# Performance work log

Measured on AMD Instinct MI355X. Metric: run time of the kernel, lower is better.

Reference implementation:

```python
import jax, jax.numpy as jnp
import numpy as np

N = 50000          # nodes
E = 1_600_000      # edges (avg degree 32)
IN = 128           # in_channels
H = 2              # heads
C = 64             # out_channels per head


def setup_inputs() -> dict:
    key = jax.random.key(0)
    k = jax.random.split(key, 6)
    x = jax.random.normal(k[0], (N, IN), dtype=jnp.float32)
    edge_index = jax.random.randint(k[1], (2, E), 0, N, dtype=jnp.int32)
    W = jax.random.normal(k[2], (IN, H * C), dtype=jnp.float32) / np.sqrt(IN).astype(np.float32)
    att_src = jax.random.normal(k[3], (H, C), dtype=jnp.float32) * 0.1
    att_dst = jax.random.normal(k[4], (H, C), dtype=jnp.float32) * 0.1
    bias = jnp.zeros((C,), dtype=jnp.float32)
    return {"x": x, "W": W, "att_src": att_src, "att_dst": att_dst,
            "bias": bias, "edge_index": edge_index}


def reference(x, W, att_src, att_dst, bias, edge_index):
    Nn = x.shape[0]
    # linear projection per head: [N, H, C]
    h = (x @ W).reshape(Nn, H, C)
    # PyG GATConv default: add self loops
    loops = jnp.arange(Nn, dtype=edge_index.dtype)
    src = jnp.concatenate([edge_index[0], loops])  # [E+N]
    dst = jnp.concatenate([edge_index[1], loops])
    # per-node attention logits: a_src . h, a_dst . h -> [N, H]
    a_s = jnp.sum(h * att_src, axis=-1)
    a_d = jnp.sum(h * att_dst, axis=-1)
    # per-edge score, leaky relu (slope 0.2)
    e = jax.nn.leaky_relu(a_s[src] + a_d[dst], 0.2)  # [E+N, H]
    # softmax over incoming edges per destination node
    emax = jax.lax.stop_gradient(jax.ops.segment_max(e, dst, num_segments=Nn))
    e = jnp.exp(e - emax[dst])
    esum = jax.ops.segment_sum(e, dst, num_segments=Nn)
    alpha = e / (esum[dst] + 1e-16)                  # [E+N, H]
    # attention-weighted message passing: scatter-sum to destinations
    out = jax.ops.segment_sum(h[src] * alpha[:, :, None], dst, num_segments=Nn)  # [N, H, C]
    # concat=False -> mean over heads, then bias
    return out.mean(axis=1) + bias  # [N, C]
```

## Files before the change

### kernel.cpp

```cpp
#include <hip/hip_runtime.h>
#include <hip/hip_bf16.h>


#define NBLK 256
#define TH 512
#define BSH 7
#define BSZ 128
#define MAXBUCK 512
#define PLCAP 8192

typedef __attribute__((ext_vector_type(8))) short bf16x8;
typedef __attribute__((ext_vector_type(4))) float f32x4;

__device__ __forceinline__ ushort f2bf(float f) {
  __hip_bfloat16 b = __float2bfloat16(f);
  union { __hip_bfloat16 b; ushort u; } cv; cv.b = b; return cv.u;
}
__device__ __forceinline__ uint pk2(float a, float b) {
  return (uint)f2bf(a) | ((uint)f2bf(b) << 16);
}

__global__ __launch_bounds__(128) void k_wa(const float* __restrict__ W,
                                            const float* __restrict__ as,
                                            const float* __restrict__ ad,
                                            ushort* __restrict__ wa) {
  const int k = threadIdx.x;
  float s0 = 0.f, s1 = 0.f, d0 = 0.f, d1 = 0.f;
  const float* wr = &W[k * 128];
  for (int c = 0; c < 64; ++c) {
    float w0 = wr[c], w1 = wr[64 + c];
    s0 = fmaf(w0, as[c], s0);
    s1 = fmaf(w1, as[64 + c], s1);
    d0 = fmaf(w0, ad[c], d0);
    d1 = fmaf(w1, ad[64 + c], d1);
  }
  wa[k * 4 + 0] = f2bf(s0);
  wa[k * 4 + 1] = f2bf(s1);
  wa[k * 4 + 2] = f2bf(d0);
  wa[k * 4 + 3] = f2bf(d1);
}

__global__ __launch_bounds__(256) void k_gemm(
    const float* __restrict__ x, const float* __restrict__ W,
    const ushort* __restrict__ wa, __hip_bfloat162* __restrict__ h2,
    float* __restrict__ a_s, float* __restrict__ a_d, int Nn) {
  __shared__ ushort Al[64 * 128];
  char* lb = (char*)Al;
  const int wave = threadIdx.x >> 6;
  const int lane = threadIdx.x & 63;
  const int row0 = blockIdx.x * 64;
  const int l15 = lane & 15;
  const int kb = (lane >> 4) * 8;

  {
    const int t = threadIdx.x;
    const int srow = t >> 2, q = t & 3;
    int gr = row0 + srow; gr = (gr < Nn) ? gr : (Nn - 1);
    const float4* xr = (const float4*)&x[(size_t)gr * 128 + q * 32];
#pragma unroll
    for (int i = 0; i < 4; ++i) {
      float4 v0 = xr[2 * i], v1 = xr[2 * i + 1];
      uint4 w;
      w.x = pk2(v0.x, v0.y); w.y = pk2(v0.z, v0.w);
      w.z = pk2(v1.x, v1.y); w.w = pk2(v1.z, v1.w);
      int byte = srow * 256 + ((q * 64 + i * 16) ^ ((srow & 7) << 4));
      *(uint4*)(lb + byte) = w;
    }
  }

  bf16x8 bfr[2][4];
#pragma unroll
  for (int c = 0; c < 2; ++c) {
#pragma unroll
    for (int ks = 0; ks < 4; ++ks) {
      const float* wp = &W[(ks * 32 + kb) * 128 + wave * 32 + c * 16 + l15];
      union { bf16x8 v; ushort u[8]; } t;
#pragma unroll
      for (int j = 0; j < 8; ++j) t.u[j] = f2bf(wp[j * 128]);
      bfr[c][ks] = t.v;
    }
  }
  bf16x8 wafr[4];
  if (wave == 3) {
#pragma unroll
    for (int ks = 0; ks < 4; ++ks) {
      union { bf16x8 v; ushort u[8]; } t;
#pragma unroll
      for (int j = 0; j < 8; ++j)
        t.u[j] = (l15 < 4) ? wa[(ks * 32 + kb + j) * 4 + l15] : (ushort)0;
      wafr[ks] = t.v;
    }
  }

  __syncthreads();

  f32x4 acc[4][2];
  f32x4 accwa[4];
#pragma unroll
  for (int r = 0; r < 4; ++r) {
    acc[r][0] = (f32x4){0.f, 0.f, 0.f, 0.f};
    acc[r][1] = (f32x4){0.f, 0.f, 0.f, 0.f};
    accwa[r] = (f32x4){0.f, 0.f, 0.f, 0.f};
  }
#pragma unroll
  for (int ks = 0; ks < 4; ++ks) {
    bf16x8 af[4];
#pragma unroll
    for (int r = 0; r < 4; ++r) {
      int row = r * 16 + l15;
      int byte = row * 256 + ((ks * 64 + (lane >> 4) * 16) ^ ((row & 7) << 4));
      uint4 v = *(const uint4*)(lb + byte);
      union { uint4 q; bf16x8 v; } cv; cv.q = v;
      af[r] = cv.v;
    }
#pragma unroll
    for (int r = 0; r < 4; ++r) {
      acc[r][0] = __builtin_amdgcn_mfma_f32_16x16x32_bf16(af[r], bfr[0][ks],
                                                          acc[r][0], 0, 0, 0);
      acc[r][1] = __builtin_amdgcn_mfma_f32_16x16x32_bf16(af[r], bfr[1][ks],
                                                          acc[r][1], 0, 0, 0);
    }
    if (wave == 3) {
#pragma unroll
      for (int r = 0; r < 4; ++r)
        accwa[r] = __builtin_amdgcn_mfma_f32_16x16x32_bf16(af[r], wafr[ks],
                                                           accwa[r], 0, 0, 0);
    }
  }

  ushort* hs = (ushort*)h2;
  const int rbase = (lane >> 4) * 4;
#pragma unroll
  for (int r = 0; r < 4; ++r) {
#pragma unroll
    for (int c = 0; c < 2; ++c) {
      int col = wave * 32 + c * 16 + l15;
#pragma unroll
      for (int i = 0; i < 4; ++i) {
        int grow = row0 + r * 16 + rbase + i;
        if (grow < Nn) hs[(size_t)grow * 128 + col] = f2bf(acc[r][c][i]);
      }
    }
  }
  if (wave == 3) {
#pragma unroll
    for (int r = 0; r < 4; ++r) {
#pragma unroll
      for (int i = 0; i < 4; ++i) {
        int grow = row0 + r * 16 + rbase + i;
        if (grow < Nn) {
          float v = accwa[r][i];
          if (l15 < 2) a_s[grow * 2 + l15] = v;
          else if (l15 < 4) a_d[grow * 2 + (l15 - 2)] = v;
        }
      }
    }
  }
}

__global__ __launch_bounds__(TH) void k_bhist(const int* __restrict__ dst,
                                              int* __restrict__ bhist, int E,
                                              int nbuck, int chunk) {
  __shared__ int hl[MAXBUCK];
  for (int i = threadIdx.x; i < nbuck; i += TH) hl[i] = 0;
  __syncthreads();
  const int s = blockIdx.x * chunk;
  const int e = (s + chunk < E) ? s + chunk : E;
  for (int i = s + threadIdx.x; i < e; i += TH)
    atomicAdd(&hl[dst[i] >> BSH], 1);
  __syncthreads();
  for (int b = threadIdx.x; b < nbuck; b += TH)
    bhist[b * NBLK + blockIdx.x] = hl[b];
}

__global__ __launch_bounds__(NBLK) void k_bscan(const int* __restrict__ bhist,
                                                int* __restrict__ cursors,
                                                int* __restrict__ totals,
                                                int nbuck) {
  __shared__ int tmp[NBLK];
  const int b = blockIdx.x;
  const int t = threadIdx.x;
  const int v = bhist[b * NBLK + t];
  tmp[t] = v;
  __syncthreads();
  for (int d = 1; d < NBLK; d <<= 1) {
    int add = (t >= d) ? tmp[t - d] : 0;
    __syncthreads();
    tmp[t] += add;
    __syncthreads();
  }
  cursors[t * nbuck + b] = tmp[t] - v;
  if (t == NBLK - 1) totals[b] = tmp[t];
}

__global__ __launch_bounds__(MAXBUCK) void k_bbase(const int* __restrict__ totals,
                                                   int* __restrict__ bases,
                                                   int nbuck) {
  __shared__ int tmp[MAXBUCK];
  const int t = threadIdx.x;
  const int v = (t < nbuck) ? totals[t] : 0;
  tmp[t] = v;
  __syncthreads();
  for (int d = 1; d < MAXBUCK; d <<= 1) {
    int add = (t >= d) ? tmp[t - d] : 0;
    __syncthreads();
    tmp[t] += add;
    __syncthreads();
  }
  if (t < nbuck) bases[t] = tmp[t] - v;
  if (t == nbuck - 1) bases[nbuck] = tmp[t];
}

__global__ __launch_bounds__(TH) void k_binsert(
    const int* __restrict__ src, const int* __restrict__ dst,
    const int* __restrict__ cursors, const int* __restrict__ bases,
    int* __restrict__ pairs, int E, int nbuck, int chunk) {
  __shared__ int cur[MAXBUCK];
  for (int i = threadIdx.x; i < nbuck; i += TH)
    cur[i] = cursors[blockIdx.x * nbuck + i] + bases[i];
  __syncthreads();
  const int s = blockIdx.x * chunk;
  const int e = (s + chunk < E) ? s + chunk : E;
  for (int i = s + threadIdx.x; i < e; i += TH) {
    const int d = dst[i];
    const int b = d >> BSH;
    const int p = atomicAdd(&cur[b], 1);
    pairs[p] = ((d & (BSZ - 1)) << 16) | src[i];
  }
}

__global__ __launch_bounds__(256) void k_bucket(
    const int* __restrict__ pairs, const int* __restrict__ bases,
    int* __restrict__ off, int* __restrict__ cnt, int* __restrict__ csr,
    int Nn) {
  __shared__ int pl[PLCAP];
  __shared__ int cl[BSZ];
  __shared__ int tmp[BSZ];
  __shared__ int cu[BSZ];
  const int b = blockIdx.x;
  const int t = threadIdx.x;
  const int n0 = b << BSH;
  if (t < BSZ) cl[t] = 0;
  __syncthreads();
  const int s = bases[b], e = bases[b + 1];
  const int len = e - s;
  const bool fit = (len <= PLCAP);
  if (fit) {
    for (int i = t; i < len; i += 256) {
      int pv = pairs[s + i];
      pl[i] = pv;
      atomicAdd(&cl[pv >> 16], 1);
    }
  } else {
    for (int i = s + t; i < e; i += 256) atomicAdd(&cl[pairs[i] >> 16], 1);
  }
  __syncthreads();
  int v = 0;
  if (t < BSZ) { v = cl[t]; tmp[t] = v; }
  __syncthreads();
  for (int d = 1; d < BSZ; d <<= 1) {
    int add = (t < BSZ && t >= d) ? tmp[t - d] : 0;
    __syncthreads();
    if (t < BSZ) tmp[t] += add;
    __syncthreads();
  }
  if (t < BSZ) {
    const int excl = tmp[t] - v;
    cu[t] = s + excl;
    const int node = n0 + t;
    if (node < Nn) { off[node] = s + excl; cnt[node] = v; }
  }
  __syncthreads();
  if (fit) {
    for (int i = t; i < len; i += 256) {
      const int pv = pl[i];
      const int p = atomicAdd(&cu[pv >> 16], 1);
      csr[p] = pv & 0xffff;
    }
  } else {
    for (int i = s + t; i < e; i += 256) {
      const int pv = pairs[i];
      const int p = atomicAdd(&cu[pv >> 16], 1);
      csr[p] = pv & 0xffff;
    }
  }
}

__device__ __forceinline__ float leaky02(float v) {
  return fmaxf(v, 0.2f * v);
}

__global__ __launch_bounds__(256) void k_aggr(
    const __hip_bfloat162* __restrict__ h2, const float* __restrict__ a_s,
    const float* __restrict__ a_d, const int* __restrict__ off,
    const int* __restrict__ cnt, const int* __restrict__ csr,
    const float* __restrict__ bias, float* __restrict__ out, int Nn) {
  __shared__ uint2 ewA[4][64];
  __shared__ uint2 ewB[4][64];
  const int wave = threadIdx.x >> 6;
  const int lane = threadIdx.x & 63;
  const int d = blockIdx.x * 4 + wave;
  if (d >= Nn) return;
  const int o = off[d];
  const int deg = cnt[d];
  const float2 ad2 = *(const float2*)&a_d[d * 2];
  const char* hb = (const char*)h2;
  const unsigned l4 = lane * 4u;
  const uint4* ebase = (lane < 32) ? (const uint4*)&ewA[wave][0]
                                   : (const uint4*)&ewB[wave][0];

  float acc0 = 0.f, acc1 = 0.f;
  float sw0 = 0.f, sw1 = 0.f;

  for (int c = 0; c < deg; c += 64) {
    int rem = deg - c; if (rem > 64) rem = 64;
    {
      unsigned voff = 0; float w0 = 0.f, w1 = 0.f;
      if (lane < rem) {
        int sl = csr[o + c + lane];
        float2 as2 = *(const float2*)&a_s[sl * 2];
        w0 = __expf(leaky02(as2.x + ad2.x));
        w1 = __expf(leaky02(as2.y + ad2.y));
        voff = (unsigned)sl << 8;
        sw0 += w0; sw1 += w1;
      }
      ewA[wave][lane] = make_uint2(voff, __float_as_uint(w0));
      ewB[wave][lane] = make_uint2(voff, __float_as_uint(w1));
    }
    const int nq = (rem + 1) >> 1;
    int q = 0;
    for (; q + 4 <= nq; q += 4) {
      uint4 p0 = ebase[q + 0];
      uint4 p1 = ebase[q + 1];
      uint4 p2 = ebase[q + 2];
      uint4 p3 = ebase[q + 3];
      __hip_bfloat162 hA0 = *(const __hip_bfloat162*)(hb + (size_t)(p0.x + l4));
      __hip_bfloat162 hB0 = *(const __hip_bfloat162*)(hb + (size_t)(p0.z + l4));
      __hip_bfloat162 hA1 = *(const __hip_bfloat162*)(hb + (size_t)(p1.x + l4));
      __hip_bfloat162 hB1 = *(const __hip_bfloat162*)(hb + (size_t)(p1.z + l4));
      __hip_bfloat162 hA2 = *(const __hip_bfloat162*)(hb + (size_t)(p2.x + l4));
      __hip_bfloat162 hB2 = *(const __hip_bfloat162*)(hb + (size_t)(p2.z + l4));
      __hip_bfloat162 hA3 = *(const __hip_bfloat162*)(hb + (size_t)(p3.x + l4));
      __hip_bfloat162 hB3 = *(const __hip_bfloat162*)(hb + (size_t)(p3.z + l4));
      acc0 = fmaf(__uint_as_float(p0.y), __bfloat162float(hA0.x), acc0);
      acc1 = fmaf(__uint_as_float(p0.y), __bfloat162float(hA0.y), acc1);
      acc0 = fmaf(__uint_as_float(p0.w), __bfloat162float(hB0.x), acc0);
      acc1 = fmaf(__uint_as_float(p0.w), __bfloat162float(hB0.y), acc1);
      acc0 = fmaf(__uint_as_float(p1.y), __bfloat162float(hA1.x), acc0);
      acc1 = fmaf(__uint_as_float(p1.y), __bfloat162float(hA1.y), acc1);
      acc0 = fmaf(__uint_as_float(p1.w), __bfloat162float(hB1.x), acc0);
      acc1 = fmaf(__uint_as_float(p1.w), __bfloat162float(hB1.y), acc1);
      acc0 = fmaf(__uint_as_float(p2.y), __bfloat162float(hA2.x), acc0);
      acc1 = fmaf(__uint_as_float(p2.y), __bfloat162float(hA2.y), acc1);
      acc0 = fmaf(__uint_as_float(p2.w), __bfloat162float(hB2.x), acc0);
      acc1 = fmaf(__uint_as_float(p2.w), __bfloat162float(hB2.y), acc1);
      acc0 = fmaf(__uint_as_float(p3.y), __bfloat162float(hA3.x), acc0);
      acc1 = fmaf(__uint_as_float(p3.y), __bfloat162float(hA3.y), acc1);
      acc0 = fmaf(__uint_as_float(p3.w), __bfloat162float(hB3.x), acc0);
      acc1 = fmaf(__uint_as_float(p3.w), __bfloat162float(hB3.y), acc1);
    }
    for (; q < nq; ++q) {
      uint4 p = ebase[q];
      __hip_bfloat162 hA = *(const __hip_bfloat162*)(hb + (size_t)(p.x + l4));
      __hip_bfloat162 hB = *(const __hip_bfloat162*)(hb + (size_t)(p.z + l4));
      acc0 = fmaf(__uint_as_float(p.y), __bfloat162float(hA.x), acc0);
      acc1 = fmaf(__uint_as_float(p.y), __bfloat162float(hA.y), acc1);
      acc0 = fmaf(__uint_as_float(p.w), __bfloat162float(hB.x), acc0);
      acc1 = fmaf(__uint_as_float(p.w), __bfloat162float(hB.y), acc1);
    }
  }
#pragma unroll
  for (int msk = 1; msk <= 32; msk <<= 1) {
    sw0 += __shfl_xor(sw0, msk, 64);
    sw1 += __shfl_xor(sw1, msk, 64);
  }
  {
    float2 as2 = *(const float2*)&a_s[d * 2];
    float w0 = __expf(leaky02(as2.x + ad2.x));
    float w1 = __expf(leaky02(as2.y + ad2.y));
    sw0 += w0; sw1 += w1;
    float av = (lane < 32) ? w0 : w1;
    __hip_bfloat162 hv = h2[(size_t)d * 64 + lane];
    acc0 = fmaf(av, __bfloat162float(hv.x), acc0);
    acc1 = fmaf(av, __bfloat162float(hv.y), acc1);
  }
  const float invsel = 1.f / (((lane < 32) ? sw0 : sw1) + 1e-16f);
  acc0 *= invsel; acc1 *= invsel;
  float o0 = acc0 + __shfl_down(acc0, 32, 64);
  float o1 = acc1 + __shfl_down(acc1, 32, 64);
  if (lane < 32) {
    int c = lane * 2;
    float2 res = make_float2(0.5f * o0 + bias[c], 0.5f * o1 + bias[c + 1]);
    *(float2*)&out[(size_t)d * 64 + c] = res;
  }
}

extern "C" void kernel_launch(void* const* d_in, const int* in_sizes, int n_in,
                              void* d_out, int out_size, void* d_ws,
                              size_t ws_size, hipStream_t stream) {
  const float* x = (const float*)d_in[0];
  const float* W = (const float*)d_in[1];
  const float* att_s = (const float*)d_in[2];
  const float* att_d = (const float*)d_in[3];
  const float* bias = (const float*)d_in[4];
  const int* ei = (const int*)d_in[5];
  const int Nn = in_sizes[0] / 128;
  const int E = in_sizes[5] / 2;
  const int* src = ei;
  const int* dst = ei + E;
  float* out = (float*)d_out;

  const int nbuck = (Nn + BSZ - 1) >> BSH;
  const int chunk = (E + NBLK - 1) / NBLK;

  __hip_bfloat162* h2 = (__hip_bfloat162*)d_ws;
  float* a_s = (float*)(h2 + (size_t)Nn * 64);
  float* a_d = a_s + (size_t)Nn * 2;
  int* off = (int*)(a_d + (size_t)Nn * 2);
  int* cnt = off + Nn;
  int* bhist = cnt + Nn;
  int* cursors = bhist + (size_t)nbuck * NBLK;
  int* totals = cursors + (size_t)NBLK * nbuck;
  int* bases = totals + nbuck;
  ushort* wa = (ushort*)(bases + nbuck + 1);
  int* pairs = (int*)(wa + 512);
  int* csr = pairs + (size_t)E;

  hipLaunchKernelGGL(k_wa, dim3(1), dim3(128), 0, stream, W, att_s, att_d, wa);
  hipLaunchKernelGGL(k_gemm, dim3((Nn + 63) / 64), dim3(256), 0, stream, x, W,
                     wa, h2, a_s, a_d, Nn);
  hipLaunchKernelGGL(k_bhist, dim3(NBLK), dim3(TH), 0, stream, dst, bhist, E,
                     nbuck, chunk);
  hipLaunchKernelGGL(k_bscan, dim3(nbuck), dim3(NBLK), 0, stream, bhist,
                     cursors, totals, nbuck);
  hipLaunchKernelGGL(k_bbase, dim3(1), dim3(MAXBUCK), 0, stream, totals, bases,
                     nbuck);
  hipLaunchKernelGGL(k_binsert, dim3(NBLK), dim3(TH), 0, stream, src, dst,
                     cursors, bases, pairs, E, nbuck, chunk);
  hipLaunchKernelGGL(k_bucket, dim3(nbuck), dim3(256), 0, stream, pairs, bases,
                     off, cnt, csr, Nn);
  hipLaunchKernelGGL(k_aggr, dim3((Nn + 3) / 4), dim3(256), 0, stream, h2, a_s,
                     a_d, off, cnt, csr, bias, out, Nn);
}
```

Baseline: 117.8 us.

## Split aggregation into alpha precompute and column-split gather with atomic output

Replaces the single fused aggregation kernel with three kernels: an output init with bias, a kernel that computes normalized attention weights per edge (including the self loop) into two per-head edge arrays, and a gather kernel launched over four column quarters that accumulates weighted bf16 features and atomically adds into the output. The aim is more parallelism and memory-level concurrency in the gather, since each wave handles 4 edges at a time over 16-lane groups. The cost is extra global writes and reads of the edge weight arrays (16 bytes per edge), each edge's exp being computed twice, one more launch, and atomic adds on the output.

```diff
diff --git a/kernel.cpp b/kernel.cpp
--- a/kernel.cpp
+++ b/kernel.cpp
@@ -290,108 +290,110 @@
   return fmaxf(v, 0.2f * v);
 }
 
-__global__ __launch_bounds__(256) void k_aggr(
-    const __hip_bfloat162* __restrict__ h2, const float* __restrict__ a_s,
-    const float* __restrict__ a_d, const int* __restrict__ off,
-    const int* __restrict__ cnt, const int* __restrict__ csr,
-    const float* __restrict__ bias, float* __restrict__ out, int Nn) {
-  __shared__ uint2 ewA[4][64];
-  __shared__ uint2 ewB[4][64];
+__global__ __launch_bounds__(256) void k_init(float* __restrict__ out,
+                                              const float* __restrict__ bias,
+                                              int total) {
+  int i = blockIdx.x * 256 + threadIdx.x;
+  if (i < total) out[i] = bias[i & 63];
+}
+
+__global__ __launch_bounds__(256) void k_alpha(
+    const float* __restrict__ a_s, const float* __restrict__ a_d,
+    const int* __restrict__ off, const int* __restrict__ cnt,
+    const int* __restrict__ csr, uint2* __restrict__ ed0,
+    uint2* __restrict__ ed1, int Nn) {
   const int wave = threadIdx.x >> 6;
   const int lane = threadIdx.x & 63;
   const int d = blockIdx.x * 4 + wave;
   if (d >= Nn) return;
-  const int o = off[d];
-  const int deg = cnt[d];
+  const int o = off[d], deg = cnt[d];
+  const int o2 = o + d;
   const float2 ad2 = *(const float2*)&a_d[d * 2];
-  const char* hb = (const char*)h2;
-  const unsigned l4 = lane * 4u;
-  const uint4* ebase = (lane < 32) ? (const uint4*)&ewA[wave][0]
-                                   : (const uint4*)&ewB[wave][0];
-
-  float acc0 = 0.f, acc1 = 0.f;
   float sw0 = 0.f, sw1 = 0.f;
-
-  for (int c = 0; c < deg; c += 64) {
-    int rem = deg - c; if (rem > 64) rem = 64;
-    {
-      unsigned voff = 0; float w0 = 0.f, w1 = 0.f;
-      if (lane < rem) {
-        int sl = csr[o + c + lane];
-        float2 as2 = *(const float2*)&a_s[sl * 2];
-        w0 = __expf(leaky02(as2.x + ad2.x));
-        w1 = __expf(leaky02(as2.y + ad2.y));
-        voff = (unsigned)sl << 8;
-        sw0 += w0; sw1 += w1;
-      }
-      ewA[wave][lane] = make_uint2(voff, __float_as_uint(w0));
-      ewB[wave][lane] = make_uint2(voff, __float_as_uint(w1));
-    }
-    const int nq = (rem + 1) >> 1;
-    int q = 0;
-    for (; q + 4 <= nq; q += 4) {
-      uint4 p0 = ebase[q + 0];
-      uint4 p1 = ebase[q + 1];
-      uint4 p2 = ebase[q + 2];
-      uint4 p3 = ebase[q + 3];
-      __hip_bfloat162 hA0 = *(const __hip_bfloat162*)(hb + (size_t)(p0.x + l4));
-      __hip_bfloat162 hB0 = *(const __hip_bfloat162*)(hb + (size_t)(p0.z + l4));
-      __hip_bfloat162 hA1 = *(const __hip_bfloat162*)(hb + (size_t)(p1.x + l4));
-      __hip_bfloat162 hB1 = *(const __hip_bfloat162*)(hb + (size_t)(p1.z + l4));
-      __hip_bfloat162 hA2 = *(const __hip_bfloat162*)(hb + (size_t)(p2.x + l4));
-      __hip_bfloat162 hB2 = *(const __hip_bfloat162*)(hb + (size_t)(p2.z + l4));
-      __hip_bfloat162 hA3 = *(const __hip_bfloat162*)(hb + (size_t)(p3.x + l4));
-      __hip_bfloat162 hB3 = *(const __hip_bfloat162*)(hb + (size_t)(p3.z + l4));
-      acc0 = fmaf(__uint_as_float(p0.y), __bfloat162float(hA0.x), acc0);
-      acc1 = fmaf(__uint_as_float(p0.y), __bfloat162float(hA0.y), acc1);
-      acc0 = fmaf(__uint_as_float(p0.w), __bfloat162float(hB0.x), acc0);
-      acc1 = fmaf(__uint_as_float(p0.w), __bfloat162float(hB0.y), acc1);
-      acc0 = fmaf(__uint_as_float(p1.y), __bfloat162float(hA1.x), acc0);
-      acc1 = fmaf(__uint_as_float(p1.y), __bfloat162float(hA1.y), acc1);
-      acc0 = fmaf(__uint_as_float(p1.w), __bfloat162float(hB1.x), acc0);
-      acc1 = fmaf(__uint_as_float(p1.w), __bfloat162float(hB1.y), acc1);
-      acc0 = fmaf(__uint_as_float(p2.y), __bfloat162float(hA2.x), acc0);
-      acc1 = fmaf(__uint_as_float(p2.y), __bfloat162float(hA2.y), acc1);
-      acc0 = fmaf(__uint_as_float(p2.w), __bfloat162float(hB2.x), acc0);
-      acc1 = fmaf(__uint_as_float(p2.w), __bfloat162float(hB2.y), acc1);
-      acc0 = fmaf(__uint_as_float(p3.y), __bfloat162float(hA3.x), acc0);
-      acc1 = fmaf(__uint_as_float(p3.y), __bfloat162float(hA3.y), acc1);
-      acc0 = fmaf(__uint_as_float(p3.w), __bfloat162float(hB3.x), acc0);
-      acc1 = fmaf(__uint_as_float(p3.w), __bfloat162float(hB3.y), acc1);
-    }
-    for (; q < nq; ++q) {
-      uint4 p = ebase[q];
-      __hip_bfloat162 hA = *(const __hip_bfloat162*)(hb + (size_t)(p.x + l4));
-      __hip_bfloat162 hB = *(const __hip_bfloat162*)(hb + (size_t)(p.z + l4));
-      acc0 = fmaf(__uint_as_float(p.y), __bfloat162float(hA.x), acc0);
-      acc1 = fmaf(__uint_as_float(p.y), __bfloat162float(hA.y), acc1);
-      acc0 = fmaf(__uint_as_float(p.w), __bfloat162float(hB.x), acc0);
-      acc1 = fmaf(__uint_as_float(p.w), __bfloat162float(hB.y), acc1);
-    }
-  }
-#pragma unroll
-  for (int msk = 1; msk <= 32; msk <<= 1) {
-    sw0 += __shfl_xor(sw0, msk, 64);
-    sw1 += __shfl_xor(sw1, msk, 64);
-  }
-  {
-    float2 as2 = *(const float2*)&a_s[d * 2];
+  for (int e = lane; e < deg; e += 64) {
+    int sl = csr[o + e];
+    float2 as2 = *(const float2*)&a_s[sl * 2];
+    sw0 += __expf(leaky02(as2.x + ad2.x));
+    sw1 += __expf(leaky02(as2.y + ad2.y));
+  }
+#pragma unroll
+  for (int m = 1; m <= 32; m <<= 1) {
+    sw0 += __shfl_xor(sw0, m, 64);
+    sw1 += __shfl_xor(sw1, m, 64);
+  }
+  const float2 asd = *(const float2*)&a_s[d * 2];
+  const float ws0 = __expf(leaky02(asd.x + ad2.x));
+  const float ws1 = __expf(leaky02(asd.y + ad2.y));
+  const float inv0 = 1.f / (sw0 + ws0 + 1e-16f);
+  const float inv1 = 1.f / (sw1 + ws1 + 1e-16f);
+  for (int e = lane; e < deg; e += 64) {
+    int sl = csr[o + e];
+    float2 as2 = *(const float2*)&a_s[sl * 2];
     float w0 = __expf(leaky02(as2.x + ad2.x));
     float w1 = __expf(leaky02(as2.y + ad2.y));
-    sw0 += w0; sw1 += w1;
-    float av = (lane < 32) ? w0 : w1;
-    __hip_bfloat162 hv = h2[(size_t)d * 64 + lane];
-    acc0 = fmaf(av, __bfloat162float(hv.x), acc0);
-    acc1 = fmaf(av, __bfloat162float(hv.y), acc1);
-  }
-  const float invsel = 1.f / (((lane < 32) ? sw0 : sw1) + 1e-16f);
-  acc0 *= invsel; acc1 *= invsel;
-  float o0 = acc0 + __shfl_down(acc0, 32, 64);
-  float o1 = acc1 + __shfl_down(acc1, 32, 64);
-  if (lane < 32) {
-    int c = lane * 2;
-    float2 res = make_float2(0.5f * o0 + bias[c], 0.5f * o1 + bias[c + 1]);
-    *(float2*)&out[(size_t)d * 64 + c] = res;
+    ed0[o2 + e] = make_uint2((uint)sl << 8, __float_as_uint(w0 * inv0));
+    ed1[o2 + e] = make_uint2((uint)sl << 8, __float_as_uint(w1 * inv1));
+  }
+  if (lane == 0) {
+    ed0[o2 + deg] = make_uint2((uint)d << 8, __float_as_uint(ws0 * inv0));
+    ed1[o2 + deg] = make_uint2((uint)d << 8, __float_as_uint(ws1 * inv1));
+  }
+}
+
+__global__ __launch_bounds__(256) void k_gat(
+    const __hip_bfloat162* __restrict__ h2, const uint2* __restrict__ ed0,
+    const uint2* __restrict__ ed1, const int* __restrict__ off,
+    const int* __restrict__ cnt, float* __restrict__ out, int Nn) {
+  const int wave = threadIdx.x >> 6;
+  const int lane = threadIdx.x & 63;
+  const int d = blockIdx.x * 4 + wave;
+  if (d >= Nn) return;
+  const int c = blockIdx.y;
+  const uint2* __restrict__ ed = (c >> 1) ? ed1 : ed0;
+  const int n = cnt[d] + 1;
+  const int o2 = off[d] + d;
+  const char* hb = (const char*)h2;
+  const uint claneoff =
+      (uint)((c >> 1) * 128 + (c & 1) * 64 + (lane & 15) * 4);
+  const int g = lane >> 4;
+  float acc0 = 0.f, acc1 = 0.f;
+  int e = 0;
+  for (; e + 16 <= n; e += 16) {
+    uint2 e0 = ed[o2 + e + g];
+    uint2 e1 = ed[o2 + e + 4 + g];
+    uint2 e2 = ed[o2 + e + 8 + g];
+    uint2 e3 = ed[o2 + e + 12 + g];
+    uint v0 = *(const uint*)(hb + (size_t)(e0.x + claneoff));
+    uint v1 = *(const uint*)(hb + (size_t)(e1.x + claneoff));
+    uint v2 = *(const uint*)(hb + (size_t)(e2.x + claneoff));
+    uint v3 = *(const uint*)(hb + (size_t)(e3.x + claneoff));
+    float a0 = __uint_as_float(e0.y), a1 = __uint_as_float(e1.y);
+    float a2 = __uint_as_float(e2.y), a3 = __uint_as_float(e3.y);
+    acc0 = fmaf(a0, __uint_as_float(v0 << 16), acc0);
+    acc1 = fmaf(a0, __uint_as_float(v0 & 0xffff0000u), acc1);
+    acc0 = fmaf(a1, __uint_as_float(v1 << 16), acc0);
+    acc1 = fmaf(a1, __uint_as_float(v1 & 0xffff0000u), acc1);
+    acc0 = fmaf(a2, __uint_as_float(v2 << 16), acc0);
+    acc1 = fmaf(a2, __uint_as_float(v2 & 0xffff0000u), acc1);
+    acc0 = fmaf(a3, __uint_as_float(v3 << 16), acc0);
+    acc1 = fmaf(a3, __uint_as_float(v3 & 0xffff0000u), acc1);
+  }
+  for (; e < n; e += 4) {
+    int idx = e + g;
+    uint2 e0 = ed[o2 + ((idx < n) ? idx : n - 1)];
+    float a0 = (idx < n) ? __uint_as_float(e0.y) : 0.f;
+    uint v0 = *(const uint*)(hb + (size_t)(e0.x + claneoff));
+    acc0 = fmaf(a0, __uint_as_float(v0 << 16), acc0);
+    acc1 = fmaf(a0, __uint_as_float(v0 & 0xffff0000u), acc1);
+  }
+  acc0 += __shfl_xor(acc0, 16, 64);
+  acc0 += __shfl_xor(acc0, 32, 64);
+  acc1 += __shfl_xor(acc1, 16, 64);
+  acc1 += __shfl_xor(acc1, 32, 64);
+  if (lane < 16) {
+    float* op = &out[(size_t)d * 64 + (c & 1) * 32 + lane * 2];
+    atomicAdd(op, 0.5f * acc0);
+    atomicAdd(op + 1, 0.5f * acc1);
   }
 }
 
@@ -425,6 +427,10 @@
   ushort* wa = (ushort*)(bases + nbuck + 1);
   int* pairs = (int*)(wa + 512);
   int* csr = pairs + (size_t)E;
+  uint2* ed0 = (uint2*)(csr + (size_t)E);
+  uint2* ed1 = ed0 + (size_t)(E + Nn);
+
+  const int ndb = (Nn + 3) / 4;
 
   hipLaunchKernelGGL(k_wa, dim3(1), dim3(128), 0, stream, W, att_s, att_d, wa);
   hipLaunchKernelGGL(k_gemm, dim3((Nn + 63) / 64), dim3(256), 0, stream, x, W,
@@ -439,6 +445,10 @@
                      cursors, bases, pairs, E, nbuck, chunk);
   hipLaunchKernelGGL(k_bucket, dim3(nbuck), dim3(256), 0, stream, pairs, bases,
                      off, cnt, csr, Nn);
-  hipLaunchKernelGGL(k_aggr, dim3((Nn + 3) / 4), dim3(256), 0, stream, h2, a_s,
-                     a_d, off, cnt, csr, bias, out, Nn);
-}
+  hipLaunchKernelGGL(k_init, dim3((Nn * 64 + 255) / 256), dim3(256), 0, stream,
+                     out, bias, Nn * 64);
+  hipLaunchKernelGGL(k_alpha, dim3(ndb), dim3(256), 0, stream, a_s, a_d, off,
+                     cnt, csr, ed0, ed1, Nn);
+  hipLaunchKernelGGL(k_gat, dim3(ndb, 4), dim3(256), 0, stream, h2, ed0, ed1,
+                     off, cnt, out, Nn);
+}
```

Measured after the change: 204.9 us. 1.74x slower.

## Precompute normalized attention weights in bucket kernel and stream them into aggregation

Applied to the files above, without the earlier changes.

The per-edge softmax (exp, per-destination sum, reciprocal) moves into the bucketing kernel, which now writes 16-byte records holding the source offset and the normalized weights for both heads, with the self-loop included per node. The aggregation kernel then only streams these records and gathers h, with no a_s lookups, no exp and no cross-lane reductions. It also unrolls the gather by 8 and converts bf16 with bit shifts. The cost is a larger edge array (16 B per edge instead of 4 B written and read back) and a second pass over pairs in the bucket kernel that recomputes exp and issues shared-memory float atomics.

```diff
diff --git a/kernel.cpp b/kernel.cpp
--- a/kernel.cpp
+++ b/kernel.cpp
@@ -229,30 +229,44 @@
   }
 }
 
+__device__ __forceinline__ float leaky02(float v) {
+  return fmaxf(v, 0.2f * v);
+}
+
 __global__ __launch_bounds__(256) void k_bucket(
     const int* __restrict__ pairs, const int* __restrict__ bases,
-    int* __restrict__ off, int* __restrict__ cnt, int* __restrict__ csr,
+    const float* __restrict__ a_s, const float* __restrict__ a_d,
+    int* __restrict__ off, int* __restrict__ cnt, uint4* __restrict__ edAB,
     int Nn) {
   __shared__ int pl[PLCAP];
   __shared__ int cl[BSZ];
   __shared__ int tmp[BSZ];
   __shared__ int cu[BSZ];
+  __shared__ float es0[BSZ], es1[BSZ];
+  __shared__ float inv0l[BSZ], inv1l[BSZ];
+  __shared__ float adl0[BSZ], adl1[BSZ];
   const int b = blockIdx.x;
   const int t = threadIdx.x;
   const int n0 = b << BSH;
-  if (t < BSZ) cl[t] = 0;
+  if (t < BSZ) {
+    cl[t] = 0; es0[t] = 0.f; es1[t] = 0.f;
+    const int node = n0 + t;
+    float2 ad2 = make_float2(0.f, 0.f);
+    if (node < Nn) ad2 = *(const float2*)&a_d[node * 2];
+    adl0[t] = ad2.x; adl1[t] = ad2.y;
+  }
   __syncthreads();
   const int s = bases[b], e = bases[b + 1];
   const int len = e - s;
   const bool fit = (len <= PLCAP);
-  if (fit) {
-    for (int i = t; i < len; i += 256) {
-      int pv = pairs[s + i];
-      pl[i] = pv;
-      atomicAdd(&cl[pv >> 16], 1);
-    }
-  } else {
-    for (int i = s + t; i < e; i += 256) atomicAdd(&cl[pairs[i] >> 16], 1);
+  for (int i = t; i < len; i += 256) {
+    const int pv = pairs[s + i];
+    if (fit) pl[i] = pv;
+    const int ld = pv >> 16, sr = pv & 0xffff;
+    atomicAdd(&cl[ld], 1);
+    float2 as2 = *(const float2*)&a_s[sr * 2];
+    atomicAdd(&es0[ld], __expf(leaky02(as2.x + adl0[ld])));
+    atomicAdd(&es1[ld], __expf(leaky02(as2.y + adl1[ld])));
   }
   __syncthreads();
   int v = 0;
@@ -268,32 +282,37 @@
     const int excl = tmp[t] - v;
     cu[t] = s + excl;
     const int node = n0 + t;
-    if (node < Nn) { off[node] = s + excl; cnt[node] = v; }
-  }
-  __syncthreads();
-  if (fit) {
-    for (int i = t; i < len; i += 256) {
-      const int pv = pl[i];
-      const int p = atomicAdd(&cu[pv >> 16], 1);
-      csr[p] = pv & 0xffff;
-    }
-  } else {
-    for (int i = s + t; i < e; i += 256) {
-      const int pv = pairs[i];
-      const int p = atomicAdd(&cu[pv >> 16], 1);
-      csr[p] = pv & 0xffff;
-    }
-  }
-}
-
-__device__ __forceinline__ float leaky02(float v) {
-  return fmaxf(v, 0.2f * v);
+    if (node < Nn) {
+      off[node] = s + excl;
+      cnt[node] = v;
+      float2 asd = *(const float2*)&a_s[node * 2];
+      const float ws0 = __expf(leaky02(asd.x + adl0[t]));
+      const float ws1 = __expf(leaky02(asd.y + adl1[t]));
+      const float i0 = 1.f / (es0[t] + ws0 + 1e-16f);
+      const float i1 = 1.f / (es1[t] + ws1 + 1e-16f);
+      inv0l[t] = i0; inv1l[t] = i1;
+      const size_t sidx = (size_t)(s + excl + v) + node;
+      edAB[sidx] = make_uint4((uint)node << 8, __float_as_uint(ws0 * i0),
+                              (uint)node << 8, __float_as_uint(ws1 * i1));
+    }
+  }
+  __syncthreads();
+  for (int i = t; i < len; i += 256) {
+    const int pv = fit ? pl[i] : pairs[s + i];
+    const int ld = pv >> 16, sr = pv & 0xffff;
+    float2 as2 = *(const float2*)&a_s[sr * 2];
+    const float w0 = __expf(leaky02(as2.x + adl0[ld]));
+    const float w1 = __expf(leaky02(as2.y + adl1[ld]));
+    const int p = atomicAdd(&cu[ld], 1);
+    const size_t gi = (size_t)p + (n0 + ld);
+    edAB[gi] = make_uint4((uint)sr << 8, __float_as_uint(w0 * inv0l[ld]),
+                          (uint)sr << 8, __float_as_uint(w1 * inv1l[ld]));
+  }
 }
 
 __global__ __launch_bounds__(256) void k_aggr(
-    const __hip_bfloat162* __restrict__ h2, const float* __restrict__ a_s,
-    const float* __restrict__ a_d, const int* __restrict__ off,
-    const int* __restrict__ cnt, const int* __restrict__ csr,
+    const __hip_bfloat162* __restrict__ h2, const uint4* __restrict__ edAB,
+    const int* __restrict__ off, const int* __restrict__ cnt,
     const float* __restrict__ bias, float* __restrict__ out, int Nn) {
   __shared__ uint2 ewA[4][64];
   __shared__ uint2 ewB[4][64];
@@ -301,91 +320,54 @@
   const int lane = threadIdx.x & 63;
   const int d = blockIdx.x * 4 + wave;
   if (d >= Nn) return;
-  const int o = off[d];
-  const int deg = cnt[d];
-  const float2 ad2 = *(const float2*)&a_d[d * 2];
+  const int o2 = off[d] + d;
+  const int n = cnt[d] + 1;
   const char* hb = (const char*)h2;
   const unsigned l4 = lane * 4u;
   const uint4* ebase = (lane < 32) ? (const uint4*)&ewA[wave][0]
                                    : (const uint4*)&ewB[wave][0];
-
   float acc0 = 0.f, acc1 = 0.f;
-  float sw0 = 0.f, sw1 = 0.f;
-
-  for (int c = 0; c < deg; c += 64) {
-    int rem = deg - c; if (rem > 64) rem = 64;
+
+  for (int c = 0; c < n; c += 64) {
+    int rem = n - c; if (rem > 64) rem = 64;
     {
-      unsigned voff = 0; float w0 = 0.f, w1 = 0.f;
-      if (lane < rem) {
-        int sl = csr[o + c + lane];
-        float2 as2 = *(const float2*)&a_s[sl * 2];
-        w0 = __expf(leaky02(as2.x + ad2.x));
-        w1 = __expf(leaky02(as2.y + ad2.y));
-        voff = (unsigned)sl << 8;
-        sw0 += w0; sw1 += w1;
-      }
-      ewA[wave][lane] = make_uint2(voff, __float_as_uint(w0));
-      ewB[wave][lane] = make_uint2(voff, __float_as_uint(w1));
+      uint4 tld = make_uint4(0, 0, 0, 0);
+      if (lane < rem) tld = edAB[(size_t)o2 + c + lane];
+      ewA[wave][lane] = make_uint2(tld.x, tld.y);
+      ewB[wave][lane] = make_uint2(tld.z, tld.w);
     }
     const int nq = (rem + 1) >> 1;
     int q = 0;
-    for (; q + 4 <= nq; q += 4) {
-      uint4 p0 = ebase[q + 0];
-      uint4 p1 = ebase[q + 1];
-      uint4 p2 = ebase[q + 2];
-      uint4 p3 = ebase[q + 3];
-      __hip_bfloat162 hA0 = *(const __hip_bfloat162*)(hb + (size_t)(p0.x + l4));
-      __hip_bfloat162 hB0 = *(const __hip_bfloat162*)(hb + (size_t)(p0.z + l4));
-      __hip_bfloat162 hA1 = *(const __hip_bfloat162*)(hb + (size_t)(p1.x + l4));
-      __hip_bfloat162 hB1 = *(const __hip_bfloat162*)(hb + (size_t)(p1.z + l4));
-      __hip_bfloat162 hA2 = *(const __hip_bfloat162*)(hb + (size_t)(p2.x + l4));
-      __hip_bfloat162 hB2 = *(const __hip_bfloat162*)(hb + (size_t)(p2.z + l4));
-      __hip_bfloat162 hA3 = *(const __hip_bfloat162*)(hb + (size_t)(p3.x + l4));
-      __hip_bfloat162 hB3 = *(const __hip_bfloat162*)(hb + (size_t)(p3.z + l4));
-      acc0 = fmaf(__uint_as_float(p0.y), __bfloat162float(hA0.x), acc0);
-      acc1 = fmaf(__uint_as_float(p0.y), __bfloat162float(hA0.y), acc1);
-      acc0 = fmaf(__uint_as_float(p0.w), __bfloat162float(hB0.x), acc0);
-      acc1 = fmaf(__uint_as_float(p0.w), __bfloat162float(hB0.y), acc1);
-      acc0 = fmaf(__uint_as_float(p1.y), __bfloat162float(hA1.x), acc0);
-      acc1 = fmaf(__uint_as_float(p1.y), __bfloat162float(hA1.y), acc1);
-      acc0 = fmaf(__uint_as_float(p1.w), __bfloat162float(hB1.x), acc0);
-      acc1 = fmaf(__uint_as_float(p1.w), __bfloat162float(hB1.y), acc1);
-      acc0 = fmaf(__uint_as_float(p2.y), __bfloat162float(hA2.x), acc0);
-      acc1 = fmaf(__uint_as_float(p2.y), __bfloat162float(hA2.y), acc1);
-      acc0 = fmaf(__uint_as_float(p2.w), __bfloat162float(hB2.x), acc0);
-      acc1 = fmaf(__uint_as_float(p2.w), __bfloat162float(hB2.y), acc1);
-      acc0 = fmaf(__uint_as_float(p3.y), __bfloat162float(hA3.x), acc0);
-      acc1 = fmaf(__uint_as_float(p3.y), __bfloat162float(hA3.y), acc1);
-      acc0 = fmaf(__uint_as_float(p3.w), __bfloat162float(hB3.x), acc0);
-      acc1 = fmaf(__uint_as_float(p3.w), __bfloat162float(hB3.y), acc1);
+    for (; q + 8 <= nq; q += 8) {
+      uint4 p[8];
+#pragma unroll
+      for (int u = 0; u < 8; ++u) p[u] = ebase[q + u];
+      uint va[8], vb[8];
+#pragma unroll
+      for (int u = 0; u < 8; ++u) {
+        va[u] = *(const uint*)(hb + (size_t)(p[u].x + l4));
+        vb[u] = *(const uint*)(hb + (size_t)(p[u].z + l4));
+      }
+#pragma unroll
+      for (int u = 0; u < 8; ++u) {
+        const float aa = __uint_as_float(p[u].y);
+        const float ab = __uint_as_float(p[u].w);
+        acc0 = fmaf(aa, __uint_as_float(va[u] << 16), acc0);
+        acc1 = fmaf(aa, __uint_as_float(va[u] & 0xffff0000u), acc1);
+        acc0 = fmaf(ab, __uint_as_float(vb[u] << 16), acc0);
+        acc1 = fmaf(ab, __uint_as_float(vb[u] & 0xffff0000u), acc1);
+      }
     }
     for (; q < nq; ++q) {
       uint4 p = ebase[q];
-      __hip_bfloat162 hA = *(const __hip_bfloat162*)(hb + (size_t)(p.x + l4));
-      __hip_bfloat162 hB = *(const __hip_bfloat162*)(hb + (size_t)(p.z + l4));
-      acc0 = fmaf(__uint_as_float(p.y), __bfloat162float(hA.x), acc0);
-      acc1 = fmaf(__uint_as_float(p.y), __bfloat162float(hA.y), acc1);
-      acc0 = fmaf(__uint_as_float(p.w), __bfloat162float(hB.x), acc0);
-      acc1 = fmaf(__uint_as_float(p.w), __bfloat162float(hB.y), acc1);
-    }
-  }
-#pragma unroll
-  for (int msk = 1; msk <= 32; msk <<= 1) {
-    sw0 += __shfl_xor(sw0, msk, 64);
-    sw1 += __shfl_xor(sw1, msk, 64);
-  }
-  {
-    float2 as2 = *(const float2*)&a_s[d * 2];
-    float w0 = __expf(leaky02(as2.x + ad2.x));
-    float w1 = __expf(leaky02(as2.y + ad2.y));
-    sw0 += w0; sw1 += w1;
-    float av = (lane < 32) ? w0 : w1;
-    __hip_bfloat162 hv = h2[(size_t)d * 64 + lane];
-    acc0 = fmaf(av, __bfloat162float(hv.x), acc0);
-    acc1 = fmaf(av, __bfloat162float(hv.y), acc1);
-  }
-  const float invsel = 1.f / (((lane < 32) ? sw0 : sw1) + 1e-16f);
-  acc0 *= invsel; acc1 *= invsel;
+      uint va = *(const uint*)(hb + (size_t)(p.x + l4));
+      uint vb = *(const uint*)(hb + (size_t)(p.z + l4));
+      acc0 = fmaf(__uint_as_float(p.y), __uint_as_float(va << 16), acc0);
+      acc1 = fmaf(__uint_as_float(p.y), __uint_as_float(va & 0xffff0000u), acc1);
+      acc0 = fmaf(__uint_as_float(p.w), __uint_as_float(vb << 16), acc0);
+      acc1 = fmaf(__uint_as_float(p.w), __uint_as_float(vb & 0xffff0000u), acc1);
+    }
+  }
   float o0 = acc0 + __shfl_down(acc0, 32, 64);
   float o1 = acc1 + __shfl_down(acc1, 32, 64);
   if (lane < 32) {
@@ -414,7 +396,8 @@
   const int chunk = (E + NBLK - 1) / NBLK;
 
   __hip_bfloat162* h2 = (__hip_bfloat162*)d_ws;
-  float* a_s = (float*)(h2 + (size_t)Nn * 64);
+  uint4* edAB = (uint4*)(h2 + (size_t)Nn * 64);
+  float* a_s = (float*)(edAB + (size_t)(E + Nn));
   float* a_d = a_s + (size_t)Nn * 2;
   int* off = (int*)(a_d + (size_t)Nn * 2);
   int* cnt = off + Nn;
@@ -424,7 +407,8 @@
   int* bases = totals + nbuck;
   ushort* wa = (ushort*)(bases + nbuck + 1);
   int* pairs = (int*)(wa + 512);
-  int* csr = pairs + (size_t)E;
+
+  const int ndb = (Nn + 3) / 4;
 
   hipLaunchKernelGGL(k_wa, dim3(1), dim3(128), 0, stream, W, att_s, att_d, wa);
   hipLaunchKernelGGL(k_gemm, dim3((Nn + 63) / 64), dim3(256), 0, stream, x, W,
@@ -438,7 +422,7 @@
   hipLaunchKernelGGL(k_binsert, dim3(NBLK), dim3(TH), 0, stream, src, dst,
                      cursors, bases, pairs, E, nbuck, chunk);
   hipLaunchKernelGGL(k_bucket, dim3(nbuck), dim3(256), 0, stream, pairs, bases,
-                     off, cnt, csr, Nn);
-  hipLaunchKernelGGL(k_aggr, dim3((Nn + 3) / 4), dim3(256), 0, stream, h2, a_s,
-                     a_d, off, cnt, csr, bias, out, Nn);
-}
+                     a_s, a_d, off, cnt, edAB, Nn);
+  hipLaunchKernelGGL(k_aggr, dim3(ndb), dim3(256), 0, stream, h2, edAB, off,
+                     cnt, bias, out, Nn);
+}
```

After: 141.3 us. 20.0% more time.
